# Kernel tuning notes

Hardware: AMD Instinct MI355X
Metric: run time of the kernel (lower is better)

The kernel has to match this reference:

```python
import jax, jax.numpy as jnp
import numpy as np

B, L, H, HEADS, DK = 256, 20, 128, 8, 16
NT, NR = 4, 4
CHILD, PARENT = 30001, 500
N1S, N1D, E1 = 50000, 20000, 300000
N2, E2 = 20000, 200000
T = B * L
N4D, E4 = 5000, 150000
EC2P = 8000
D2 = H // 2  # gamma=0.5 split for diachronic embedding


def _ln(x):
    m = jnp.mean(x, -1, keepdims=True)
    v = jnp.var(x, -1, keepdims=True)
    return (x - m) * jax.lax.rsqrt(v + 1e-5)


def _tmod(h, w, b):
    # temporal modulation with per-node diachronic params (activ='sin')
    return jnp.concatenate([h[..., :D2], h[..., D2:] * jnp.sin(w[..., D2:] + b[..., D2:])], -1)


def _dia(e, w, b, t):
    t = t[..., None].astype(e.dtype)
    return jnp.concatenate([e[..., :D2], e[..., D2:] * jnp.sin(w[..., D2:] * t + b[..., D2:])], -1)


def _typed(x, t, W):
    # type-conditioned linear: W [NT, in, out]; small NT -> compute all, select
    y = jnp.einsum('nh,tho->tno', x, W)
    return y[t, jnp.arange(x.shape[0])]


def _seg_softmax(s, seg, n):
    m = jax.ops.segment_max(s, seg, num_segments=n)
    m = jnp.where(jnp.isfinite(m), m, 0.0)
    ex = jnp.exp(s - m[seg])
    den = jax.ops.segment_sum(ex, seg, num_segments=n)
    return ex / jnp.maximum(den[seg], 1e-9)


def _htgt(src_h, src_t, tw, tb, eh, esrc, edst, etype, dst_h, dst_t, KW, QW, VW, OW, EW, mu):
    # relational multi-head attention on a bipartite block (HTGTLayer, pre_norm)
    nd = dst_h.shape[0]
    hs = _tmod(_ln(src_h), tw, tb)
    k = _typed(hs, src_t, KW).reshape(-1, HEADS, DK)
    v = _typed(hs, src_t, VW).reshape(-1, HEADS, DK)
    q = _typed(_ln(dst_h), dst_t, QW).reshape(nd, HEADS, DK)
    ke = k[esrc] + (eh @ EW).reshape(-1, HEADS, DK)
    score = (q[edst] * ke).sum(-1) * mu[etype] / np.float32(np.sqrt(DK))  # [E, HEADS]
    a = _seg_softmax(score, edst, nd)
    agg = jax.ops.segment_sum(a[..., None] * v[esrc], edst, num_segments=nd).reshape(nd, H)
    return _typed(agg, dst_t, OW) + dst_h


def _lstm(x, Wi, Wh, b):
    h0 = jnp.zeros((x.shape[0], H), x.dtype)
    def step(carry, xt):
        h, c = carry
        g = xt @ Wi + h @ Wh + b
        i, f, gg, o = jnp.split(g, 4, -1)
        c = jax.nn.sigmoid(f) * c + jax.nn.sigmoid(i) * jnp.tanh(gg)
        h = jax.nn.sigmoid(o) * jnp.tanh(c)
        return (h, c), h
    _, hs = jax.lax.scan(step, (h0, h0), jnp.swapaxes(x, 0, 1))
    return jnp.swapaxes(hs, 0, 1)


def _forward(seq, seq_ntype, dur, stime, etime, g1_nid, g1_ntype, g1_esrc, g1_edst, g1_etype, g1_ew,
             g2_src_sel, g2_esrc, g2_edst, g2_etype, g2_ew, tok_sel, g4_esrc, g4_edst, g4_etype, g4_ew,
             pe_p, pe_c, emb, hist_emb, edge_emb, dia_w, dia_b, t2v_w, t2v_b, exp_W, exp_b,
             lstm1_Wi, lstm1_Wh, lstm1_b, lstm2_Wi, lstm2_Wh, lstm2_b,
             convK, convQ, convV, convO, convE, convMu, ipW, iaW, skip):
    # ---- sequence module ----
    e0 = emb[seq]
    st = _dia(e0, dia_w[seq], dia_b[seq], stime)
    et = _dia(e0, dia_w[seq], dia_b[seq], etime)
    t = dur[..., None].astype(jnp.float32)
    tv = jnp.concatenate([t2v_w[:1] * t + t2v_b[:1], jnp.sin(t2v_w[1:] * t + t2v_b[1:])], -1)
    x = jax.nn.relu(jnp.concatenate([st, et, tv], -1) @ exp_W + exp_b)
    h1 = _lstm(x, lstm1_Wi, lstm1_Wh, lstm1_b)
    his = jnp.swapaxes(h1, 0, 1).reshape(T, H)  # packed (time-major) token states
    tok_id = jnp.swapaxes(seq, 0, 1).reshape(T)
    tok_nt = jnp.swapaxes(seq_ntype, 0, 1).reshape(T)
    # ---- conv1 (g2g) on block 1 ----
    sh1 = emb[g1_nid]
    xg = jax.nn.relu(_htgt(sh1, g1_ntype, dia_w[g1_nid], dia_b[g1_nid], edge_emb[g1_ew],
                           g1_esrc, g1_edst, g1_etype, sh1[:N1D], g1_ntype[:N1D],
                           convK[0], convQ[0], convV[0], convO[0], convE[0], convMu[0]))
    # ---- conv2 (g2s): graph nodes -> packed sequence tokens ----
    gnid2 = g1_nid[g2_src_sel]
    dst_h2 = xg[tok_sel] + his
    x2 = jax.nn.relu(_htgt(xg[g2_src_sel], g1_ntype[g2_src_sel], dia_w[gnid2], dia_b[gnid2], edge_emb[g2_ew],
                           g2_esrc, g2_edst, g2_etype, dst_h2, tok_nt,
                           convK[1], convQ[1], convV[1], convO[1], convE[1], convMu[1]))
    seq2 = jnp.swapaxes(x2.reshape(L, B, H), 0, 1)
    h2 = _lstm(seq2, lstm2_Wi, lstm2_Wh, lstm2_b)  # final seq_embed
    # ---- individual pooling (attn) + history push ----
    ent = jnp.swapaxes(h2, 0, 1).reshape(T, H)
    a = _typed(jnp.tanh(_typed(ent, tok_nt, ipW)), tok_nt, iaW)[:, 0]
    w = _seg_softmax(a, tok_id, CHILD)
    node_embed = jax.ops.segment_sum(w[:, None] * ent, tok_id, num_segments=CHILD)
    cnt = jax.ops.segment_sum(jnp.ones((T,), jnp.float32), tok_id, num_segments=CHILD)
    hist2 = jnp.where(cnt[:, None] > 0, node_embed, hist_emb)
    # ---- graph module: conv3, conv4 with skip-gated pull ----
    alpha = jax.nn.sigmoid(skip)[g1_ntype][:, None]
    x0 = emb[g1_nid] * alpha + hist2[g1_nid] * (1.0 - alpha)
    x3 = jax.nn.relu(_htgt(x0, g1_ntype, dia_w[g1_nid], dia_b[g1_nid], edge_emb[g1_ew],
                           g1_esrc, g1_edst, g1_etype, x0[:N1D], g1_ntype[:N1D],
                           convK[2], convQ[2], convV[2], convO[2], convE[2], convMu[2]))
    nid4 = g1_nid[:N1D]
    child_embed = _htgt(x3, g1_ntype[:N1D], dia_w[nid4], dia_b[nid4], edge_emb[g4_ew],
                        g4_esrc, g4_edst, g4_etype, x3[:N4D], g1_ntype[:N4D],
                        convK[3], convQ[3], convV[3], convO[3], convE[3], convMu[3])
    # ---- parent pooling (avg over c2p map) ----
    psum = jax.ops.segment_sum(child_embed[pe_c], pe_p, num_segments=PARENT)
    pcnt = jax.ops.segment_sum(jnp.ones((EC2P,), jnp.float32), pe_p, num_segments=PARENT)
    parent_embed = psum / jnp.maximum(pcnt, 1.0)[:, None]
    return (h2, child_embed, parent_embed)


def setup_inputs() -> dict:
    key = jax.random.key(0)
    ks = iter(jax.random.split(key, 64))
    def ri(shape, hi):
        return jax.random.randint(next(ks), shape, 0, hi, dtype=jnp.int32)
    def rn(shape, s=0.02):
        return jax.random.normal(next(ks), shape, dtype=jnp.float32) * s
    return dict(
        seq=ri((B, L), CHILD), seq_ntype=ri((B, L), NT), dur=ri((B, L), 40),
        stime=ri((B, L), 60), etime=ri((B, L), 60),
        g1_nid=ri((N1S,), CHILD), g1_ntype=ri((N1S,), NT),
        g1_esrc=ri((E1,), N1S), g1_edst=ri((E1,), N1D), g1_etype=ri((E1,), NR), g1_ew=ri((E1,), 50),
        g2_src_sel=ri((N2,), N1D), g2_esrc=ri((E2,), N2), g2_edst=ri((E2,), T),
        g2_etype=ri((E2,), NR), g2_ew=ri((E2,), 50),
        tok_sel=ri((T,), N1D),
        g4_esrc=ri((E4,), N1D), g4_edst=ri((E4,), N4D), g4_etype=ri((E4,), NR), g4_ew=ri((E4,), 50),
        pe_p=ri((EC2P,), PARENT), pe_c=ri((EC2P,), N4D),
        emb=rn((CHILD, H), 0.05), hist_emb=rn((CHILD, H), 0.05), edge_emb=rn((50, 32), 0.05),
        dia_w=rn((CHILD, H), 0.05), dia_b=rn((CHILD, H), 0.05),
        t2v_w=rn((16,), 0.1), t2v_b=rn((16,), 0.1),
        exp_W=rn((2 * H + 16, H)), exp_b=jnp.zeros((H,), jnp.float32),
        lstm1_Wi=rn((H, 4 * H)), lstm1_Wh=rn((H, 4 * H)), lstm1_b=jnp.zeros((4 * H,), jnp.float32),
        lstm2_Wi=rn((H, 4 * H)), lstm2_Wh=rn((H, 4 * H)), lstm2_b=jnp.zeros((4 * H,), jnp.float32),
        convK=rn((4, NT, H, H)), convQ=rn((4, NT, H, H)), convV=rn((4, NT, H, H)), convO=rn((4, NT, H, H)),
        convE=rn((4, 32, H)), convMu=jnp.ones((4, NR, HEADS), jnp.float32),
        ipW=rn((NT, H, H)), iaW=rn((NT, H, 1)), skip=jnp.ones((NT,), jnp.float32),
    )


def reference(seq, seq_ntype, dur, stime, etime, g1_nid, g1_ntype, g1_esrc, g1_edst, g1_etype, g1_ew,
              g2_src_sel, g2_esrc, g2_edst, g2_etype, g2_ew, tok_sel, g4_esrc, g4_edst, g4_etype, g4_ew,
              pe_p, pe_c, emb, hist_emb, edge_emb, dia_w, dia_b, t2v_w, t2v_b, exp_W, exp_b,
              lstm1_Wi, lstm1_Wh, lstm1_b, lstm2_Wi, lstm2_Wh, lstm2_b,
              convK, convQ, convV, convO, convE, convMu, ipW, iaW, skip):
    return _forward(seq, seq_ntype, dur, stime, etime, g1_nid, g1_ntype, g1_esrc, g1_edst, g1_etype, g1_ew,
                    g2_src_sel, g2_esrc, g2_edst, g2_etype, g2_ew, tok_sel, g4_esrc, g4_edst, g4_etype, g4_ew,
                    pe_p, pe_c, emb, hist_emb, edge_emb, dia_w, dia_b, t2v_w, t2v_b, exp_W, exp_b,
                    lstm1_Wi, lstm1_Wh, lstm1_b, lstm2_Wi, lstm2_Wh, lstm2_b,
                    convK, convQ, convV, convO, convE, convMu, ipW, iaW, skip)
```

## Files before the change

### kernel.cpp

```cpp
#include <hip/hip_runtime.h>
#include <math.h>

#define BB 256
#define LL 20
#define HH 128
#define NH 8
#define D2C 64
#define NTY 4
#define NRL 4
#define CHILDN 30001
#define PARENTN 500
#define N1SN 50000
#define N1DN 20000
#define E1N 300000
#define N2N 20000
#define E2N 200000
#define TT (BB*LL)
#define N4DN 5000
#define E4N 150000
#define EC2PN 8000
#define TDSTRIDE 2304

typedef __attribute__((ext_vector_type(8))) short bfrag;
typedef __attribute__((ext_vector_type(4))) float ffrag;
// ... 36 lines not shown
    const float* src = (fam==0?convK:fam==1?convV:fam==2?convQ:convO) + (size_t)lt*HH*HH;
    int j = im & 7, lane = (im>>3)&63, kc = (im>>9)&3, nt = im>>11;
    int k = kc*32 + (lane>>4)*8 + j;
    int n = nt*16 + (lane&15);
    Wsw[(size_t)m*16384 + im] = f2bf(src[k*HH+n]);
  }
  if(i < 4*16384){
    int m = i >> 14, im = i & 16383;
    const float* src = ipW + (size_t)m*HH*HH;
    int j = im & 7, lane = (im>>3)&63, kc = (im>>9)&3, nt = im>>11;
    int k = kc*32 + (lane>>4)*8 + j;
    int n = nt*16 + (lane&15);
    WswI[(size_t)m*16384 + im] = f2bf(src[k*HH+n]);
  }
  if(i < 4*50*HH){
    int layer = i/(50*HH), rr = (i/HH)%50, o = i%HH;
    const float* EWp = convE + (size_t)layer*32*HH;
    float acc = 0.f;
    for(int j=0;j<32;j++) acc += edge_emb[rr*32+j]*EWp[j*HH+o];
    EW2all[i] = acc;
  }
}

__global__ __launch_bounds__(512) void k_featx2(const int* __restrict__ seq, const int* __restrict__ dur,
                        const int* __restrict__ stime, const int* __restrict__ etime,
                        const float* __restrict__ emb, const float* __restrict__ dia_w, const float* __restrict__ dia_b,
                        const float* __restrict__ t2v_w, const float* __restrict__ t2v_b,
                        const float* __restrict__ exp_W, const float* __restrict__ exp_b, float* __restrict__ xout){
  __shared__ float feat[32*273];
  int base = blockIdx.x*32;
  int j = threadIdx.x >> 4;
  int p = threadIdx.x & 15;
  int row = base + j;
  int node = seq[row];
  float ts = (float)stime[row], te = (float)etime[row];
  const float* ep = emb + (size_t)node*HH;
  float* fr = feat + j*273;
  int o0 = p*8;
  #pragma unroll
  for(int ii=0; ii<8; ii+=4){
    int o = o0 + ii;
    float4 e = *(const float4*)(ep + o);
    float4 st = e, et = e;
    if(o >= D2C){
      float4 w = *(const float4*)(dia_w + (size_t)node*HH + o);
      float4 b = *(const float4*)(dia_b + (size_t)node*HH + o);
      st.x = e.x*__sinf(w.x*ts+b.x); st.y = e.y*__sinf(w.y*ts+b.y);
      st.z = e.z*__sinf(w.z*ts+b.z); st.w = e.w*__sinf(w.w*ts+b.w);
      et.x = e.x*__sinf(w.x*te+b.x); et.y = e.y*__sinf(w.y*te+b.y);
      et.z = e.z*__sinf(w.z*te+b.z); et.w = e.w*__sinf(w.w*te+b.w);
    }
    fr[o] = st.x; fr[o+1] = st.y; fr[o+2] = st.z; fr[o+3] = st.w;
    fr[128+o] = et.x; fr[128+o+1] = et.y; fr[128+o+2] = et.z; fr[128+o+3] = et.w;
  }
  if(p == 0){
    float td = (float)dur[row];
    #pragma unroll
    for(int i=0;i<16;i++){
      float w = t2v_w[i], b = t2v_b[i];
      fr[256+i] = (i==0) ? (w*td + b) : __sinf(w*td + b);
    }
  }
  __syncthreads();
  int oc = (threadIdx.x & 31)*4;
  int jg = threadIdx.x >> 5;
  const float* f0 = feat + (jg*2)*273;
  const float* f1 = feat + (jg*2+1)*273;
  float4 a0 = {0,0,0,0}, a1 = {0,0,0,0};
  for(int k=0;k<272;k++){
    float4 w = *(const float4*)(exp_W + (size_t)k*HH + oc);
    float x0 = f0[k], x1 = f1[k];
    a0.x += x0*w.x; a0.y += x0*w.y; a0.z += x0*w.z; a0.w += x0*w.w;
    a1.x += x1*w.x; a1.y += x1*w.y; a1.z += x1*w.z; a1.w += x1*w.w;
  }
  float4 bv = *(const float4*)(exp_b + oc);
  a0.x = fmaxf(a0.x+bv.x, 0.f); a0.y = fmaxf(a0.y+bv.y, 0.f);
  a0.z = fmaxf(a0.z+bv.z, 0.f); a0.w = fmaxf(a0.w+bv.w, 0.f);
  a1.x = fmaxf(a1.x+bv.x, 0.f); a1.y = fmaxf(a1.y+bv.y, 0.f);
  a1.z = fmaxf(a1.z+bv.z, 0.f); a1.w = fmaxf(a1.w+bv.w, 0.f);
  *(float4*)(xout + (size_t)(base + jg*2  )*HH + oc) = a0;
  *(float4*)(xout + (size_t)(base + jg*2+1)*HH + oc) = a1;
}

__global__ void k_xwi2(const float* x, const float* Wi, const float* bias, float* gpre, int rows, int perm){
  int base = blockIdx.x*16;
  __shared__ float xs[128*17];
  int tid = threadIdx.x;
  #pragma unroll
  for(int s=0;s<8;s++){
    int elem = tid + 256*s;
    int k = elem & 127, j = elem >> 7;
    int r = base + j;
    int src = r;
    if(perm) src = (r % LL)*BB + (r / LL);
    xs[k*17 + j] = (r < rows) ? x[(size_t)src*HH + k] : 0.f;
  }
  __syncthreads();
  int o4 = (tid & 127)*4;
  int ng = tid >> 7;
  float4 a[8];
  #pragma unroll
  for(int j=0;j<8;j++) a[j]=make_float4(0,0,0,0);
  for(int k=0;k<HH;k++){
    float4 w = *(const float4*)(Wi + (size_t)k*512 + o4);
    const float* xr = xs + k*17 + ng*8;
    #pragma unroll
    for(int j=0;j<8;j++){
      float xv = xr[j];
      a[j].x += xv*w.x; a[j].y += xv*w.y; a[j].z += xv*w.z; a[j].w += xv*w.w;
    }
  }
  float4 bv = *(const float4*)(bias + o4);
  #pragma unroll
  for(int j=0;j<8;j++){
    int r = base + ng*8 + j;
    if(r < rows){
      float4 v = a[j];
      v.x += bv.x; v.y += bv.y; v.z += bv.z; v.w += bv.w;
      *(float4*)(gpre + (size_t)r*512 + o4) = v;
    }
  }
}

__global__ __launch_bounds__(512, 2) void k_lstm_fused(const float* __restrict__ gpre,
                                                       const float* __restrict__ Wh,
                                                       float* __restrict__ hout,
                                                       float* __restrict__ hout2){
  int b = blockIdx.x;
  int o = threadIdx.x;
  __shared__ float hs[HH];
  __shared__ float act[512];
  float wr[HH];
  #pragma unroll
  for(int h=0;h<HH;h++) wr[h] = Wh[(size_t)h*512 + o];
  float gv[LL];
  const float* gp = gpre + (size_t)b*LL*512 + o;
  #pragma unroll
  for(int l=0;l<LL;l++) gv[l] = gp[(size_t)l*512];
  if(o < HH) hs[o] = 0.f;
  float cc = 0.f;
  int quad = o >> 7;
  __syncthreads();
  for(int l=0;l<LL;l++){
    float a0=0.f,a1=0.f,a2=0.f,a3=0.f;
    #pragma unroll
    for(int h=0;h<HH;h+=4){
      float4 hv = *(const float4*)&hs[h];
      a0 += hv.x*wr[h];   a1 += hv.y*wr[h+1];
      a2 += hv.z*wr[h+2]; a3 += hv.w*wr[h+3];
    }
    float g = gv[l] + ((a0+a1)+(a2+a3));
    act[o] = (quad==2) ? tanhfast(g) : sigfast(g);
    __syncthreads();
    if(o < HH){
      cc = act[HH+o]*cc + act[o]*act[2*HH+o];
      float hh = act[3*HH+o]*tanhfast(cc);
      hs[o] = hh;
      size_t bi = ((size_t)b*LL + l)*HH + o;
      hout[bi] = hh;
      if(hout2) hout2[bi] = hh;
    }
    __syncthreads();
  }
}

__global__ void k_scatall(const int* __restrict__ g1_nt, const int* __restrict__ seq,
                          const int* __restrict__ seq_nt, const int* __restrict__ g2_sel,
                          const int* __restrict__ g1_nid,
                          int* __restrict__ tokid, int* __restrict__ toknt, int* __restrict__ gnid2,
                          int* __restrict__ cntall,
                          int* __restrict__ idxS1, int* __restrict__ idxS2, int* __restrict__ idxS5,
                          int* __restrict__ idxS4, int* __restrict__ idxS3,
                          const int* __restrict__ e1d, int* __restrict__ icnt1, int* __restrict__ rank1,
                          const int* __restrict__ e2d, int* __restrict__ icnt2, int* __restrict__ rank2,
                          const int* __restrict__ e3d, int* __restrict__ icnt3, int* __restrict__ rank3){
  const int B1 = (N1SN+255)/256;
  const int B2 = (TT+255)/256;
  const int B3 = (N2N+255)/256;
  const int BE1 = (E1N+255)/256;
  const int BE2 = (E2N+255)/256;
  __shared__ int h[3][NTY];
  __shared__ int bs[3][NTY];
  int bx = blockIdx.x;
  if(bx < B1){
    int i = bx*256 + threadIdx.x;
    if(threadIdx.x < 3*NTY) (&h[0][0])[threadIdx.x] = 0;
    __syncthreads();
    int t = 0, r1 = 0, r2 = 0, r3 = 0;
    bool a1 = (i < N1SN), a2 = (i < N1DN), a3 = (i < N4DN);
    if(a1){
      t = g1_nt[i];
      r1 = atomicAdd(&h[0][t], 1);
      if(a2) r2 = atomicAdd(&h[1][t], 1);
      if(a3) r3 = atomicAdd(&h[2][t], 1);
    }
    __syncthreads();
    if(threadIdx.x < NTY){
      int ty = threadIdx.x;
      if(h[0][ty] > 0) bs[0][ty] = atomicAdd(&cntall[0*NTY+ty], h[0][ty]);
      if(h[1][ty] > 0) bs[1][ty] = atomicAdd(&cntall[1*NTY+ty], h[1][ty]);
      if(h[2][ty] > 0) bs[2][ty] = atomicAdd(&cntall[4*NTY+ty], h[2][ty]);
    }
    __syncthreads();
    if(a1) idxS1[t*N1SN + bs[0][t] + r1] = i;
    if(a2) idxS2[t*N1DN + bs[1][t] + r2] = i;
    if(a3) idxS5[t*N4DN + bs[2][t] + r3] = i;
  } else if(bx < B1 + B2){
    int i = (bx - B1)*256 + threadIdx.x;
    if(threadIdx.x < NTY) h[0][threadIdx.x] = 0;
    __syncthreads();
    int nt = 0, r = 0;
    bool act = (i < TT);
    if(act){
      int b = i % BB, l = i / BB;
      tokid[i] = seq[b*LL+l];
      nt = seq_nt[b*LL+l];
      toknt[i] = nt;
      r = atomicAdd(&h[0][nt], 1);
    }
    __syncthreads();
    if(threadIdx.x < NTY && h[0][threadIdx.x] > 0)
      bs[0][threadIdx.x] = atomicAdd(&cntall[3*NTY+threadIdx.x], h[0][threadIdx.x]);
    __syncthreads();
    if(act) idxS4[nt*TT + bs[0][nt] + r] = i;
  } else if(bx < B1 + B2 + B3){
    int i = (bx - B1 - B2)*256 + threadIdx.x;
    if(threadIdx.x < NTY) h[0][threadIdx.x] = 0;
    __syncthreads();
    int nt = 0, r = 0;
    bool act = (i < N2N);
    if(act){
      int s = g2_sel[i];
      gnid2[i] = g1_nid[s];
      nt = g1_nt[s];
      r = atomicAdd(&h[0][nt], 1);
    }
    __syncthreads();
    if(threadIdx.x < NTY && h[0][threadIdx.x] > 0)
      bs[0][threadIdx.x] = atomicAdd(&cntall[2*NTY+threadIdx.x], h[0][threadIdx.x]);
    __syncthreads();
    if(act) idxS3[nt*N2N + bs[0][nt] + r] = i;
  } else if(bx < B1 + B2 + B3 + BE1){
    int e = (bx - B1 - B2 - B3)*256 + threadIdx.x;
    if(e < E1N) rank1[e] = atomicAdd(&icnt1[e1d[e]], 1);
  } else if(bx < B1 + B2 + B3 + BE1 + BE2){
    int e = (bx - B1 - B2 - B3 - BE1)*256 + threadIdx.x;
    if(e < E2N) rank2[e] = atomicAdd(&icnt2[e2d[e]], 1);
  } else {
    int e = (bx - B1 - B2 - B3 - BE1 - BE2)*256 + threadIdx.x;
    if(e < E4N) rank3[e] = atomicAdd(&icnt3[e3d[e]], 1);
  }
}

__global__ void k_dst2(const int* tok_sel, const float* xg, const float* h1, float* dst2){
  int t = blockIdx.x; int o = threadIdx.x;
  int b = t % BB, l = t / BB;
  dst2[t*HH+o] = xg[tok_sel[t]*HH+o] + h1[(b*LL+l)*HH+o];
}

__global__ void k_x0(const int* nid, const int* ntype, const float* emb, const float* hist2,
                     const float* cnt, const float* hist_emb, const float* skip, float* srcbuf){
  int i = blockIdx.x; int o = threadIdx.x;
  float a = sigfast(skip[ntype[i]]);
  int nd = nid[i];
  float hv = (cnt[nd] > 0.f) ? hist2[(size_t)nd*HH+o] : hist_emb[(size_t)nd*HH+o];
  srcbuf[i*HH+o] = emb[(size_t)nd*HH+o]*a + hv*(1.f-a);
}

__global__ void k_mktiles(const int* __restrict__ cntall, int* __restrict__ tdesc, int* __restrict__ tcnt){
  __shared__ int start[3][2][NTY];
  if(threadIdx.x == 0){
    const int srcg[3] = {0,2,1};
    const int dstg[3] = {1,3,4};
    for(int c=0;c<3;c++){
      int acc = 0;
      for(int z=0;z<2;z++){
        int g = (z==0) ? srcg[c] : dstg[c];
        int zacc = 0;
        for(int t=0;t<NTY;t++){
          start[c][z][t] = acc;
          int tiles = (cntall[g*NTY+t]+31)>>5;
          acc += tiles; zacc += tiles;
        }
        tcnt[c*2+z] = zacc;
      }
    }
  }
  __syncthreads();
  const int srcg[3] = {0,2,1};
  const int dstg[3] = {1,3,4};
  for(int c=0;c<3;c++){
    for(int z=0;z<2;z++){
      int g = (z==0) ? srcg[c] : dstg[c];
      for(int t=0;t<NTY;t++){
        int tiles = (cntall[g*NTY+t]+31)>>5;
        for(int i=threadIdx.x; i<tiles; i+=blockDim.x)
          tdesc[c*TDSTRIDE + start[c][z][t] + i] = (int)(((unsigned)z<<31) | ((unsigned)t<<28) | (unsigned)(i<<5));
      }
    }
  }
}

__global__ __launch_bounds__(256) void k_gemm_kvq(
    const int* __restrict__ tdesc, const int* __restrict__ tcnt,
    const float* __restrict__ Xs, const int* __restrict__ src_nid, const int* __restrict__ smap,
    const float* __restrict__ sdia,
    const int* __restrict__ idxs, const int* __restrict__ cnts_s, int stride_s,
    const bfrag* __restrict__ WK, const bfrag* __restrict__ WV, unsigned* __restrict__ KVp,
    const float* __restrict__ Xq, const int* __restrict__ qmap,
    const int* __restrict__ idxd, const int* __restrict__ cnts_d, int stride_d,
    const bfrag* __restrict__ WQ, float* __restrict__ Qbuf){
  __shared__ float xs[32*132];
  __shared__ float mean_s[32], inv_s[32];
  __shared__ int sid[32], nid[32], xrow[32];
  int ntk = tcnt[0], ntq = tcnt[1];
  int bid = blockIdx.x;
  if(bid >= ntk + ntq) return;
  unsigned ud = (unsigned)tdesc[bid];
  int isQ = ud >> 31;
  int t = (ud >> 28) & 7;
  int base = ud & 0x0FFFFFFF;
  int tid = threadIdx.x;
  int cnt = isQ ? cnts_d[t] : cnts_s[t];
// ... 253 lines not shown
  for(int nt=0;nt<4;nt++){
    int col = (ng0+nt)*16 + col0;
    float wia = iaW[t*HH + col];
    #pragma unroll
    for(int i=0;i<4;i++) rsum[i] += tanhfast(acc[nt][i]) * wia;
  }
  #pragma unroll
  for(int i=0;i<4;i++){
    rsum[i] += __shfl_xor(rsum[i], 1, 64);
    rsum[i] += __shfl_xor(rsum[i], 2, 64);
    rsum[i] += __shfl_xor(rsum[i], 4, 64);
    rsum[i] += __shfl_xor(rsum[i], 8, 64);
  }
  if(col0 == 0){
    #pragma unroll
    for(int i=0;i<4;i++) atomicAdd(&red[rb+i], rsum[i]);
  }
  __syncthreads();
  if(tid < nn){
    int tok = sid[tid];
    float a = red[tid];
    abuf[tok] = a;
    atomicMax(&amax[tokid[tok]], fenc(a));
  }
}

__global__ void k_scan3(const int* c1, int n1, int* r1,
                        const int* c2, int n2, int* r2,
                        const int* c3, int n3, int* r3){
  __shared__ int tsum[1024];
  const int* cnt; int n; int* row_ptr;
  if(blockIdx.x == 0){ cnt=c1; n=n1; row_ptr=r1; }
  else if(blockIdx.x == 1){ cnt=c2; n=n2; row_ptr=r2; }
  else { cnt=c3; n=n3; row_ptr=r3; }
  int tid = threadIdx.x;
  int per = (n + 1023) / 1024;
  int start = tid*per; int end = min(start+per, n);
  int s = 0;
  for(int i=start;i<end;i++) s += cnt[i];
  tsum[tid] = s; __syncthreads();
  for(int off=1;off<1024;off<<=1){
    int v = (tid>=off) ? tsum[tid-off] : 0;
    __syncthreads();
    tsum[tid] += v;
    __syncthreads();
  }
  int run = (tid==0) ? 0 : tsum[tid-1];
  for(int i=start;i<end;i++){ row_ptr[i]=run; run += cnt[i]; }
  if(end == n) row_ptr[n] = run;
}
__global__ void k_fillperm3(const int* d1, const int* s1, const int* w1, const int* t1,
                            const int* rp1, const int* rk1, int2* m1,
                            const int* d2, const int* s2, const int* w2, const int* t2,
                            const int* rp2, const int* rk2, int2* m2,
                            const int* d3, const int* s3, const int* w3, const int* t3,
                            const int* rp3, const int* rk3, int2* m3){
  const int B1 = (E1N+255)/256, B2 = (E2N+255)/256;
  int bx = blockIdx.x;
  if(bx < B1){
    int e = bx*256 + threadIdx.x;
    if(e < E1N){ int pos = rp1[d1[e]] + rk1[e]; m1[pos] = make_int2(s1[e], w1[e] | (t1[e]<<16)); }
  } else if(bx < B1+B2){
    int e = (bx-B1)*256 + threadIdx.x;
    if(e < E2N){ int pos = rp2[d2[e]] + rk2[e]; m2[pos] = make_int2(s2[e], w2[e] | (t2[e]<<16)); }
  } else {
    int e = (bx-B1-B2)*256 + threadIdx.x;
    if(e < E4N){ int pos = rp3[d3[e]] + rk3[e]; m3[pos] = make_int2(s3[e], w3[e] | (t3[e]<<16)); }
  }
}

__global__ void k_attn_fused8(const int* __restrict__ row_ptr, const int2* __restrict__ meta,
                              const unsigned* __restrict__ KVp, const float* __restrict__ Qbuf,
                              const float* __restrict__ EW2, const float* __restrict__ mu,
                              float* __restrict__ Abuf){
  int d = blockIdx.x; int o = threadIdx.x;
  int r0 = row_ptr[d], r1 = row_ptr[d+1];
  __shared__ float q[HH];
  q[o] = Qbuf[(size_t)d*HH+o]*0.25f;
  __syncthreads();
  int h = o >> 4;
  float qo = q[o];
  float dn0=0.f, dn1=0.f, dn2=0.f, dn3=0.f;
  float ac0=0.f, ac1=0.f, ac2=0.f, ac3=0.f;
  int r = r0;
  for(; r+7 < r1; r += 8){
    int2 m[8]; unsigned u[8]; float e[8]; float p[8];
    #pragma unroll
    for(int j=0;j<8;j++) m[j] = meta[r+j];
    #pragma unroll
    for(int j=0;j<8;j++) u[j] = KVp[(size_t)m[j].x*HH + o];
// ... 207 lines not shown
    const bfrag* WK = WB + (size_t)( 0 + layer*4)*2048;
    const bfrag* WV = WB + (size_t)(16 + layer*4)*2048;
    const bfrag* WQ = WB + (size_t)(32 + layer*4)*2048;
    const bfrag* WO = WB + (size_t)(48 + layer*4)*2048;
    const float* MU  = convMu + (size_t)layer*NRL*NH;
    const float* EW2 = EW2all + (size_t)layer*50*HH;
    const int* td = tdesc + (size_t)cfg*TDSTRIDE;
    const int* tc = tcnt + cfg*2;
    k_gemm_kvq<<<gkvq, 256, 0, stream>>>(td, tc, src_X, src_nid, srcmap, sdia,
                                         idx_src, cnt_src, stride_src, WK, WV, KVp,
                                         q_X, q_map, idx_dst, cnt_dst, stride_dst, WQ, Qbuf);
    k_attn_fused8<<<ndst, HH, 0, stream>>>(rowp, meta, KVp, Qbuf, EW2, MU, Abuf);
    k_gemm_t5<<<gq, 256, 0, stream>>>(td, tc, Abuf, idx_dst, cnt_dst, stride_dst, WO,
                                      resid_X, r_map, outbuf, out2, relu);
  };

  k_init<<<(CHILDN*HH+255)/256, 256, 0, stream>>>(hist2, cnt, amax, aden, psum, pcnt, cntall,
                                                  icnt1, icnt2, icnt3,
                                                  dia_w, dia_b, sdia,
                                                  convK, convV, convQ, convO, Wsw,
                                                  ipW, WswI,
                                                  edge_emb, convE, EW2all);
  {
    const int B1 = (N1SN+255)/256, B2 = (TT+255)/256, B3 = (N2N+255)/256;
    const int BE1 = (E1N+255)/256, BE2 = (E2N+255)/256, BE3 = (E4N+255)/256;
    k_scatall<<<B1+B2+B3+BE1+BE2+BE3, 256, 0, stream>>>(g1_nt, seq, seq_nt, g2_sel, g1_nid,
                                            tokid, toknt, gnid2, cntall,
                                            idxS1, idxS2, idxS5, idxS4, idxS3,
                                            g1_edst, icnt1, g1rank,
                                            g2_edst, icnt2, g2rank,
                                            g4_edst, icnt3, g4rank);
  }
  k_mktiles<<<1, 256, 0, stream>>>(cntall, tdesc, tcnt);
  k_scan3<<<3, 1024, 0, stream>>>(icnt1, N1DN, g1row,
                                  icnt2, TT,   g2row,
                                  icnt3, N4DN, g4row);
  {
    const int BE1 = (E1N+255)/256, BE2 = (E2N+255)/256, BE3 = (E4N+255)/256;
    k_fillperm3<<<BE1+BE2+BE3, 256, 0, stream>>>(g1_edst, g1_esrc, g1_ew, g1_ety, g1row, g1rank, g1meta,
                                                 g2_edst, g2_esrc, g2_ew, g2_ety, g2row, g2rank, g2meta,
                                                 g4_edst, g4_esrc, g4_ew, g4_ety, g4row, g4rank, g4meta);
  }

  k_featx2<<<TT/32, 512, 0, stream>>>(seq, dur, stime, etime, emb, dia_w, dia_b, t2v_w, t2v_b, exp_W, exp_b, xbuf);
  k_xwi2<<<(TT+15)/16, 256, 0, stream>>>(xbuf, l1Wi, l1b, gpre, TT, 0);
  k_lstm_fused<<<BB, 512, 0, stream>>>(gpre, l1Wh, h1, (float*)nullptr);

  const int GKVQ_A = (N1SN+N1DN)/32 + 8;
  const int GKVQ_B = (N2N+TT)/32 + 8;
  const int GKVQ_C = (N1DN+N4DN)/32 + 8;
  const int GQ_A   = (N1DN+31)/32 + 4;
  const int GQ_B   = (TT+31)/32 + 4;
  const int GQ_C   = (N4DN+31)/32 + 4;

  run_conv(0, GKVQ_A, GQ_A,
           emb, g1_nid, g1_nid, idxS1, cntall+0*NTY, N1SN,
           emb, g1_nid,
           emb, g1_nid, N1DN, idxS2, cntall+1*NTY, N1DN,
           g1row, g1meta, 0, xg, (float*)nullptr, 1);

  k_dst2<<<TT, HH, 0, stream>>>(tok_sel, xg, h1, dst2);
  run_conv(1, GKVQ_B, GQ_B,
           xg, gnid2, g2_sel, idxS3, cntall+2*NTY, N2N,
           dst2, (const int*)nullptr,
           dst2, (const int*)nullptr, TT, idxS4, cntall+3*NTY, TT,
           g2row, g2meta, 1, x2, (float*)nullptr, 1);

  k_xwi2<<<(TT+15)/16, 256, 0, stream>>>(x2, l2Wi, l2b, gpre, TT, 1);
  k_lstm_fused<<<BB, 512, 0, stream>>>(gpre, l2Wh, h2f, outp);

  k_tokatt2<<<GQ_B, 256, 0, stream>>>(tdesc + (size_t)1*TDSTRIDE, tcnt + 2,
                                      h2f, idxS4, cntall+3*NTY,
                                      (const bfrag*)WswI, iaW, tokid, abuf, amax);
  k_tokexp<<<(TT+255)/256, 256, 0, stream>>>(tokid, abuf, amax, aden, cnt);
  k_tokagg<<<TT, HH, 0, stream>>>(tokid, abuf, aden, h2f, hist2);

  k_x0<<<N1SN, HH, 0, stream>>>(g1_nid, g1_nt, emb, hist2, cnt, hist_emb, skip, srcbuf);
  run_conv(0, GKVQ_A, GQ_A,
           srcbuf, g1_nid, (const int*)nullptr, idxS1, cntall+0*NTY, N1SN,
           srcbuf, (const int*)nullptr,
           srcbuf, (const int*)nullptr, N1DN, idxS2, cntall+1*NTY, N1DN,
           g1row, g1meta, 2, x3, (float*)nullptr, 1);

  run_conv(2, GKVQ_C, GQ_C,
           x3, g1_nid, (const int*)nullptr, idxS2, cntall+1*NTY, N1DN,
           x3, (const int*)nullptr,
           x3, (const int*)nullptr, N4DN, idxS5, cntall+4*NTY, N4DN,
           g4row, g4meta, 3, cef, outp + (size_t)TT*HH, 0);

  k_peagg<<<EC2PN, HH, 0, stream>>>(pe_p, pe_c, cef, psum, pcnt);
  k_parent<<<PARENTN, HH, 0, stream>>>(psum, pcnt, outp + (size_t)TT*HH + (size_t)N4DN*HH);
}
// ... 1 lines not shown
```

Measured before the change: 678.9 us.

## Merge independent preprocessing kernels into fewer multi-role launches

Folds the feature/expansion kernel and the index-scatter kernel into one launch, the input-projection GEMM together with the row-pointer scans and tile-descriptor build into a second, and the CSR fill into extra blocks of the first LSTM launch. This reduces the kernel launch count and the serialization gaps between small kernels by running independent work side by side. The scan now uses 256 threads instead of 1024, and the scatter blocks process 512 elements each. The mixed-role blocks share register and LDS budgets, which could lower occupancy for the heavier roles.

New measurement: 672.9 us. No clear change (-0.9%).

```diff
diff --git a/kernel.cpp b/kernel.cpp
--- a/kernel.cpp
+++ b/kernel.cpp
@@ -82,168 +82,90 @@
   }
 }
 
-__global__ __launch_bounds__(512) void k_featx2(const int* __restrict__ seq, const int* __restrict__ dur,
-                        const int* __restrict__ stime, const int* __restrict__ etime,
-                        const float* __restrict__ emb, const float* __restrict__ dia_w, const float* __restrict__ dia_b,
-                        const float* __restrict__ t2v_w, const float* __restrict__ t2v_b,
-                        const float* __restrict__ exp_W, const float* __restrict__ exp_b, float* __restrict__ xout){
-  __shared__ float feat[32*273];
-  int base = blockIdx.x*32;
-  int j = threadIdx.x >> 4;
-  int p = threadIdx.x & 15;
-  int row = base + j;
-  int node = seq[row];
-  float ts = (float)stime[row], te = (float)etime[row];
-  const float* ep = emb + (size_t)node*HH;
-  float* fr = feat + j*273;
-  int o0 = p*8;
-  #pragma unroll
-  for(int ii=0; ii<8; ii+=4){
-    int o = o0 + ii;
-    float4 e = *(const float4*)(ep + o);
-    float4 st = e, et = e;
-    if(o >= D2C){
-      float4 w = *(const float4*)(dia_w + (size_t)node*HH + o);
-      float4 b = *(const float4*)(dia_b + (size_t)node*HH + o);
-      st.x = e.x*__sinf(w.x*ts+b.x); st.y = e.y*__sinf(w.y*ts+b.y);
-      st.z = e.z*__sinf(w.z*ts+b.z); st.w = e.w*__sinf(w.w*ts+b.w);
-      et.x = e.x*__sinf(w.x*te+b.x); et.y = e.y*__sinf(w.y*te+b.y);
-      et.z = e.z*__sinf(w.z*te+b.z); et.w = e.w*__sinf(w.w*te+b.w);
-    }
-    fr[o] = st.x; fr[o+1] = st.y; fr[o+2] = st.z; fr[o+3] = st.w;
-    fr[128+o] = et.x; fr[128+o+1] = et.y; fr[128+o+2] = et.z; fr[128+o+3] = et.w;
-  }
-  if(p == 0){
-    float td = (float)dur[row];
-    #pragma unroll
-    for(int i=0;i<16;i++){
-      float w = t2v_w[i], b = t2v_b[i];
-      fr[256+i] = (i==0) ? (w*td + b) : __sinf(w*td + b);
-    }
-  }
-  __syncthreads();
-  int oc = (threadIdx.x & 31)*4;
-  int jg = threadIdx.x >> 5;
-  const float* f0 = feat + (jg*2)*273;
-  const float* f1 = feat + (jg*2+1)*273;
-  float4 a0 = {0,0,0,0}, a1 = {0,0,0,0};
-  for(int k=0;k<272;k++){
-    float4 w = *(const float4*)(exp_W + (size_t)k*HH + oc);
-    float x0 = f0[k], x1 = f1[k];
-    a0.x += x0*w.x; a0.y += x0*w.y; a0.z += x0*w.z; a0.w += x0*w.w;
-    a1.x += x1*w.x; a1.y += x1*w.y; a1.z += x1*w.z; a1.w += x1*w.w;
-  }
-  float4 bv = *(const float4*)(exp_b + oc);
-  a0.x = fmaxf(a0.x+bv.x, 0.f); a0.y = fmaxf(a0.y+bv.y, 0.f);
-  a0.z = fmaxf(a0.z+bv.z, 0.f); a0.w = fmaxf(a0.w+bv.w, 0.f);
-  a1.x = fmaxf(a1.x+bv.x, 0.f); a1.y = fmaxf(a1.y+bv.y, 0.f);
-  a1.z = fmaxf(a1.z+bv.z, 0.f); a1.w = fmaxf(a1.w+bv.w, 0.f);
-  *(float4*)(xout + (size_t)(base + jg*2  )*HH + oc) = a0;
-  *(float4*)(xout + (size_t)(base + jg*2+1)*HH + oc) = a1;
-}
-
-__global__ void k_xwi2(const float* x, const float* Wi, const float* bias, float* gpre, int rows, int perm){
-  int base = blockIdx.x*16;
-  __shared__ float xs[128*17];
-  int tid = threadIdx.x;
-  #pragma unroll
-  for(int s=0;s<8;s++){
-    int elem = tid + 256*s;
-    int k = elem & 127, j = elem >> 7;
-    int r = base + j;
-    int src = r;
-    if(perm) src = (r % LL)*BB + (r / LL);
-    xs[k*17 + j] = (r < rows) ? x[(size_t)src*HH + k] : 0.f;
-  }
-  __syncthreads();
-  int o4 = (tid & 127)*4;
-  int ng = tid >> 7;
-  float4 a[8];
-  #pragma unroll
-  for(int j=0;j<8;j++) a[j]=make_float4(0,0,0,0);
-  for(int k=0;k<HH;k++){
-    float4 w = *(const float4*)(Wi + (size_t)k*512 + o4);
-    const float* xr = xs + k*17 + ng*8;
-    #pragma unroll
-    for(int j=0;j<8;j++){
-      float xv = xr[j];
-      a[j].x += xv*w.x; a[j].y += xv*w.y; a[j].z += xv*w.z; a[j].w += xv*w.w;
-    }
-  }
-  float4 bv = *(const float4*)(bias + o4);
-  #pragma unroll
-  for(int j=0;j<8;j++){
-    int r = base + ng*8 + j;
-    if(r < rows){
-      float4 v = a[j];
-      v.x += bv.x; v.y += bv.y; v.z += bv.z; v.w += bv.w;
-      *(float4*)(gpre + (size_t)r*512 + o4) = v;
-    }
-  }
-}
-
-__global__ __launch_bounds__(512, 2) void k_lstm_fused(const float* __restrict__ gpre,
-                                                       const float* __restrict__ Wh,
-                                                       float* __restrict__ hout,
-                                                       float* __restrict__ hout2){
-  int b = blockIdx.x;
-  int o = threadIdx.x;
-  __shared__ float hs[HH];
-  __shared__ float act[512];
-  float wr[HH];
-  #pragma unroll
-  for(int h=0;h<HH;h++) wr[h] = Wh[(size_t)h*512 + o];
-  float gv[LL];
-  const float* gp = gpre + (size_t)b*LL*512 + o;
-  #pragma unroll
-  for(int l=0;l<LL;l++) gv[l] = gp[(size_t)l*512];
-  if(o < HH) hs[o] = 0.f;
-  float cc = 0.f;
-  int quad = o >> 7;
-  __syncthreads();
-  for(int l=0;l<LL;l++){
-    float a0=0.f,a1=0.f,a2=0.f,a3=0.f;
-    #pragma unroll
-    for(int h=0;h<HH;h+=4){
-      float4 hv = *(const float4*)&hs[h];
-      a0 += hv.x*wr[h];   a1 += hv.y*wr[h+1];
-      a2 += hv.z*wr[h+2]; a3 += hv.w*wr[h+3];
-    }
-    float g = gv[l] + ((a0+a1)+(a2+a3));
-    act[o] = (quad==2) ? tanhfast(g) : sigfast(g);
-    __syncthreads();
-    if(o < HH){
-      cc = act[HH+o]*cc + act[o]*act[2*HH+o];
-      float hh = act[3*HH+o]*tanhfast(cc);
-      hs[o] = hh;
-      size_t bi = ((size_t)b*LL + l)*HH + o;
-      hout[bi] = hh;
-      if(hout2) hout2[bi] = hh;
-    }
-    __syncthreads();
-  }
-}
-
-__global__ void k_scatall(const int* __restrict__ g1_nt, const int* __restrict__ seq,
-                          const int* __restrict__ seq_nt, const int* __restrict__ g2_sel,
-                          const int* __restrict__ g1_nid,
-                          int* __restrict__ tokid, int* __restrict__ toknt, int* __restrict__ gnid2,
-                          int* __restrict__ cntall,
-                          int* __restrict__ idxS1, int* __restrict__ idxS2, int* __restrict__ idxS5,
-                          int* __restrict__ idxS4, int* __restrict__ idxS3,
-                          const int* __restrict__ e1d, int* __restrict__ icnt1, int* __restrict__ rank1,
-                          const int* __restrict__ e2d, int* __restrict__ icnt2, int* __restrict__ rank2,
-                          const int* __restrict__ e3d, int* __restrict__ icnt3, int* __restrict__ rank3){
-  const int B1 = (N1SN+255)/256;
-  const int B2 = (TT+255)/256;
-  const int B3 = (N2N+255)/256;
-  const int BE1 = (E1N+255)/256;
-  const int BE2 = (E2N+255)/256;
+#define S1_BF   (TT/32)
+#define S1_B1   ((N1SN+511)/512)
+#define S1_B2   ((TT+511)/512)
+#define S1_B3   ((N2N+511)/512)
+#define S1_BE1  ((E1N+511)/512)
+#define S1_BE2  ((E2N+511)/512)
+#define S1_BE3  ((E4N+511)/512)
+__global__ __launch_bounds__(512) void k_stage1(
+    const int* __restrict__ seq, const int* __restrict__ dur,
+    const int* __restrict__ stime, const int* __restrict__ etime,
+    const float* __restrict__ emb, const float* __restrict__ dia_w, const float* __restrict__ dia_b,
+    const float* __restrict__ t2v_w, const float* __restrict__ t2v_b,
+    const float* __restrict__ exp_W, const float* __restrict__ exp_b, float* __restrict__ xout,
+    const int* __restrict__ g1_nt, const int* __restrict__ seq_nt, const int* __restrict__ g2_sel,
+    const int* __restrict__ g1_nid,
+    int* __restrict__ tokid, int* __restrict__ toknt, int* __restrict__ gnid2,
+    int* __restrict__ cntall,
+    int* __restrict__ idxS1, int* __restrict__ idxS2, int* __restrict__ idxS5,
+    int* __restrict__ idxS4, int* __restrict__ idxS3,
+    const int* __restrict__ e1d, int* __restrict__ icnt1, int* __restrict__ rank1,
+    const int* __restrict__ e2d, int* __restrict__ icnt2, int* __restrict__ rank2,
+    const int* __restrict__ e3d, int* __restrict__ icnt3, int* __restrict__ rank3){
+  int bxx = blockIdx.x;
+  if(bxx < S1_BF){
+    __shared__ float feat[32*273];
+    int base = bxx*32;
+    int j = threadIdx.x >> 4;
+    int p = threadIdx.x & 15;
+    int row = base + j;
+    int node = seq[row];
+    float ts = (float)stime[row], te = (float)etime[row];
+    const float* ep = emb + (size_t)node*HH;
+    float* fr = feat + j*273;
+    int o0 = p*8;
+    #pragma unroll
+    for(int ii=0; ii<8; ii+=4){
+      int o = o0 + ii;
+      float4 e = *(const float4*)(ep + o);
+      float4 st = e, et = e;
+      if(o >= D2C){
+        float4 w = *(const float4*)(dia_w + (size_t)node*HH + o);
+        float4 b = *(const float4*)(dia_b + (size_t)node*HH + o);
+        st.x = e.x*__sinf(w.x*ts+b.x); st.y = e.y*__sinf(w.y*ts+b.y);
+        st.z = e.z*__sinf(w.z*ts+b.z); st.w = e.w*__sinf(w.w*ts+b.w);
+        et.x = e.x*__sinf(w.x*te+b.x); et.y = e.y*__sinf(w.y*te+b.y);
+        et.z = e.z*__sinf(w.z*te+b.z); et.w = e.w*__sinf(w.w*te+b.w);
+      }
+      fr[o] = st.x; fr[o+1] = st.y; fr[o+2] = st.z; fr[o+3] = st.w;
+      fr[128+o] = et.x; fr[128+o+1] = et.y; fr[128+o+2] = et.z; fr[128+o+3] = et.w;
+    }
+    if(p == 0){
+      float td = (float)dur[row];
+      #pragma unroll
+      for(int i=0;i<16;i++){
+        float w = t2v_w[i], b = t2v_b[i];
+        fr[256+i] = (i==0) ? (w*td + b) : __sinf(w*td + b);
+      }
+    }
+    __syncthreads();
+    int oc = (threadIdx.x & 31)*4;
+    int jg = threadIdx.x >> 5;
+    const float* f0 = feat + (jg*2)*273;
+    const float* f1 = feat + (jg*2+1)*273;
+    float4 a0 = {0,0,0,0}, a1 = {0,0,0,0};
+    for(int k=0;k<272;k++){
+      float4 w = *(const float4*)(exp_W + (size_t)k*HH + oc);
+      float x0 = f0[k], x1 = f1[k];
+      a0.x += x0*w.x; a0.y += x0*w.y; a0.z += x0*w.z; a0.w += x0*w.w;
+      a1.x += x1*w.x; a1.y += x1*w.y; a1.z += x1*w.z; a1.w += x1*w.w;
+    }
+    float4 bv = *(const float4*)(exp_b + oc);
+    a0.x = fmaxf(a0.x+bv.x, 0.f); a0.y = fmaxf(a0.y+bv.y, 0.f);
+    a0.z = fmaxf(a0.z+bv.z, 0.f); a0.w = fmaxf(a0.w+bv.w, 0.f);
+    a1.x = fmaxf(a1.x+bv.x, 0.f); a1.y = fmaxf(a1.y+bv.y, 0.f);
+    a1.z = fmaxf(a1.z+bv.z, 0.f); a1.w = fmaxf(a1.w+bv.w, 0.f);
+    *(float4*)(xout + (size_t)(base + jg*2  )*HH + oc) = a0;
+    *(float4*)(xout + (size_t)(base + jg*2+1)*HH + oc) = a1;
+    return;
+  }
   __shared__ int h[3][NTY];
   __shared__ int bs[3][NTY];
-  int bx = blockIdx.x;
-  if(bx < B1){
-    int i = bx*256 + threadIdx.x;
+  int bx = bxx - S1_BF;
+  if(bx < S1_B1){
+    int i = bx*512 + threadIdx.x;
     if(threadIdx.x < 3*NTY) (&h[0][0])[threadIdx.x] = 0;
     __syncthreads();
     int t = 0, r1 = 0, r2 = 0, r3 = 0;
@@ -265,8 +187,8 @@
     if(a1) idxS1[t*N1SN + bs[0][t] + r1] = i;
     if(a2) idxS2[t*N1DN + bs[1][t] + r2] = i;
     if(a3) idxS5[t*N4DN + bs[2][t] + r3] = i;
-  } else if(bx < B1 + B2){
-    int i = (bx - B1)*256 + threadIdx.x;
+  } else if(bx < S1_B1 + S1_B2){
+    int i = (bx - S1_B1)*512 + threadIdx.x;
     if(threadIdx.x < NTY) h[0][threadIdx.x] = 0;
     __syncthreads();
     int nt = 0, r = 0;
@@ -283,8 +205,8 @@
       bs[0][threadIdx.x] = atomicAdd(&cntall[3*NTY+threadIdx.x], h[0][threadIdx.x]);
     __syncthreads();
     if(act) idxS4[nt*TT + bs[0][nt] + r] = i;
-  } else if(bx < B1 + B2 + B3){
-    int i = (bx - B1 - B2)*256 + threadIdx.x;
+  } else if(bx < S1_B1 + S1_B2 + S1_B3){
+    int i = (bx - S1_B1 - S1_B2)*512 + threadIdx.x;
     if(threadIdx.x < NTY) h[0][threadIdx.x] = 0;
     __syncthreads();
     int nt = 0, r = 0;
@@ -300,15 +222,185 @@
       bs[0][threadIdx.x] = atomicAdd(&cntall[2*NTY+threadIdx.x], h[0][threadIdx.x]);
     __syncthreads();
     if(act) idxS3[nt*N2N + bs[0][nt] + r] = i;
-  } else if(bx < B1 + B2 + B3 + BE1){
-    int e = (bx - B1 - B2 - B3)*256 + threadIdx.x;
+  } else if(bx < S1_B1 + S1_B2 + S1_B3 + S1_BE1){
+    int e = (bx - S1_B1 - S1_B2 - S1_B3)*512 + threadIdx.x;
     if(e < E1N) rank1[e] = atomicAdd(&icnt1[e1d[e]], 1);
-  } else if(bx < B1 + B2 + B3 + BE1 + BE2){
-    int e = (bx - B1 - B2 - B3 - BE1)*256 + threadIdx.x;
+  } else if(bx < S1_B1 + S1_B2 + S1_B3 + S1_BE1 + S1_BE2){
+    int e = (bx - S1_B1 - S1_B2 - S1_B3 - S1_BE1)*512 + threadIdx.x;
     if(e < E2N) rank2[e] = atomicAdd(&icnt2[e2d[e]], 1);
   } else {
-    int e = (bx - B1 - B2 - B3 - BE1 - BE2)*256 + threadIdx.x;
+    int e = (bx - S1_B1 - S1_B2 - S1_B3 - S1_BE1 - S1_BE2)*512 + threadIdx.x;
     if(e < E4N) rank3[e] = atomicAdd(&icnt3[e3d[e]], 1);
+  }
+}
+
+__device__ __forceinline__ void scan_one(const int* cnt, int n, int* row_ptr){
+  __shared__ int tsum[256];
+  int tid = threadIdx.x;
+  int per = (n + 255) / 256;
+  int start = tid*per; int end = min(start+per, n);
+  int s = 0;
+  for(int i=start;i<end;i++) s += cnt[i];
+  tsum[tid] = s; __syncthreads();
+  for(int off=1;off<256;off<<=1){
+    int v = (tid>=off) ? tsum[tid-off] : 0;
+    __syncthreads();
+    tsum[tid] += v;
+    __syncthreads();
+  }
+  int run = (tid==0) ? 0 : tsum[tid-1];
+  for(int i=start;i<end;i++){ row_ptr[i]=run; run += cnt[i]; }
+  if(end == n) row_ptr[n] = run;
+}
+
+__global__ __launch_bounds__(256) void k_stage2(
+    const float* x, const float* Wi, const float* bias, float* gpre, int rows, int perm,
+    const int* c1, int* r1, const int* c2, int* r2, const int* c3, int* r3,
+    const int* __restrict__ cntall, int* __restrict__ tdesc, int* __restrict__ tcnt){
+  int nxwi = (rows+15)/16;
+  int bxx = blockIdx.x;
+  if(bxx < nxwi){
+    int base = bxx*16;
+    __shared__ float xs[128*17];
+    int tid = threadIdx.x;
+    #pragma unroll
+    for(int s=0;s<8;s++){
+      int elem = tid + 256*s;
+      int k = elem & 127, j = elem >> 7;
+      int r = base + j;
+      int src = r;
+      if(perm) src = (r % LL)*BB + (r / LL);
+      xs[k*17 + j] = (r < rows) ? x[(size_t)src*HH + k] : 0.f;
+    }
+    __syncthreads();
+    int o4 = (tid & 127)*4;
+    int ng = tid >> 7;
+    float4 a[8];
+    #pragma unroll
+    for(int j=0;j<8;j++) a[j]=make_float4(0,0,0,0);
+    for(int k=0;k<HH;k++){
+      float4 w = *(const float4*)(Wi + (size_t)k*512 + o4);
+      const float* xr = xs + k*17 + ng*8;
+      #pragma unroll
+      for(int j=0;j<8;j++){
+        float xv = xr[j];
+        a[j].x += xv*w.x; a[j].y += xv*w.y; a[j].z += xv*w.z; a[j].w += xv*w.w;
+      }
+    }
+    float4 bv = *(const float4*)(bias + o4);
+    #pragma unroll
+    for(int j=0;j<8;j++){
+      int r = base + ng*8 + j;
+      if(r < rows){
+        float4 v = a[j];
+        v.x += bv.x; v.y += bv.y; v.z += bv.z; v.w += bv.w;
+        *(float4*)(gpre + (size_t)r*512 + o4) = v;
+      }
+    }
+    return;
+  }
+  int bx = bxx - nxwi;
+  if(bx == 0){ scan_one(c1, N1DN, r1); }
+  else if(bx == 1){ scan_one(c2, TT, r2); }
+  else if(bx == 2){ scan_one(c3, N4DN, r3); }
+  else {
+    __shared__ int start[3][2][NTY];
+    if(threadIdx.x == 0){
+      const int srcg[3] = {0,2,1};
+      const int dstg[3] = {1,3,4};
+      for(int c=0;c<3;c++){
+        int acc = 0;
+        for(int z=0;z<2;z++){
+          int g = (z==0) ? srcg[c] : dstg[c];
+          int zacc = 0;
+          for(int t=0;t<NTY;t++){
+            start[c][z][t] = acc;
+            int tiles = (cntall[g*NTY+t]+31)>>5;
+            acc += tiles; zacc += tiles;
+          }
+          tcnt[c*2+z] = zacc;
+        }
+      }
+    }
+    __syncthreads();
+    const int srcg[3] = {0,2,1};
+    const int dstg[3] = {1,3,4};
+    for(int c=0;c<3;c++){
+      for(int z=0;z<2;z++){
+        int g = (z==0) ? srcg[c] : dstg[c];
+        for(int t=0;t<NTY;t++){
+          int tiles = (cntall[g*NTY+t]+31)>>5;
+          for(int i=threadIdx.x; i<tiles; i+=blockDim.x)
+            tdesc[c*TDSTRIDE + start[c][z][t] + i] = (int)(((unsigned)z<<31) | ((unsigned)t<<28) | (unsigned)(i<<5));
+        }
+      }
+    }
+  }
+}
+
+#define LF_BE1 ((E1N+511)/512)
+#define LF_BE2 ((E2N+511)/512)
+#define LF_BE3 ((E4N+511)/512)
+__global__ __launch_bounds__(512, 2) void k_lstm_fused(const float* __restrict__ gpre,
+                                                       const float* __restrict__ Wh,
+                                                       float* __restrict__ hout,
+                                                       float* __restrict__ hout2,
+    const int* d1, const int* s1, const int* w1, const int* t1,
+    const int* rp1, const int* rk1, int2* m1,
+    const int* d2, const int* s2, const int* w2, const int* t2,
+    const int* rp2, const int* rk2, int2* m2,
+    const int* d3, const int* s3, const int* w3, const int* t3,
+    const int* rp3, const int* rk3, int2* m3){
+  if(blockIdx.x >= BB){
+    int bx = blockIdx.x - BB;
+    int tid = threadIdx.x;
+    if(bx < LF_BE1){
+      int e = bx*512 + tid;
+      if(e < E1N){ int pos = rp1[d1[e]] + rk1[e]; m1[pos] = make_int2(s1[e], w1[e] | (t1[e]<<16)); }
+    } else if(bx < LF_BE1 + LF_BE2){
+      int e = (bx - LF_BE1)*512 + tid;
+      if(e < E2N){ int pos = rp2[d2[e]] + rk2[e]; m2[pos] = make_int2(s2[e], w2[e] | (t2[e]<<16)); }
+    } else {
+      int e = (bx - LF_BE1 - LF_BE2)*512 + tid;
+      if(e < E4N){ int pos = rp3[d3[e]] + rk3[e]; m3[pos] = make_int2(s3[e], w3[e] | (t3[e]<<16)); }
+    }
+    return;
+  }
+  int b = blockIdx.x;
+  int o = threadIdx.x;
+  __shared__ float hs[HH];
+  __shared__ float act[512];
+  float wr[HH];
+  #pragma unroll
+  for(int h=0;h<HH;h++) wr[h] = Wh[(size_t)h*512 + o];
+  float gv[LL];
+  const float* gp = gpre + (size_t)b*LL*512 + o;
+  #pragma unroll
+  for(int l=0;l<LL;l++) gv[l] = gp[(size_t)l*512];
+  if(o < HH) hs[o] = 0.f;
+  float cc = 0.f;
+  int quad = o >> 7;
+  __syncthreads();
+  for(int l=0;l<LL;l++){
+    float a0=0.f,a1=0.f,a2=0.f,a3=0.f;
+    #pragma unroll
+    for(int h=0;h<HH;h+=4){
+      float4 hv = *(const float4*)&hs[h];
+      a0 += hv.x*wr[h];   a1 += hv.y*wr[h+1];
+      a2 += hv.z*wr[h+2]; a3 += hv.w*wr[h+3];
+    }
+    float g = gv[l] + ((a0+a1)+(a2+a3));
+    act[o] = (quad==2) ? tanhfast(g) : sigfast(g);
+    __syncthreads();
+    if(o < HH){
+      cc = act[HH+o]*cc + act[o]*act[2*HH+o];
+      float hh = act[3*HH+o]*tanhfast(cc);
+      hs[o] = hh;
+      size_t bi = ((size_t)b*LL + l)*HH + o;
+      hout[bi] = hh;
+      if(hout2) hout2[bi] = hh;
+    }
+    __syncthreads();
   }
 }
 
@@ -325,40 +417,6 @@
   int nd = nid[i];
   float hv = (cnt[nd] > 0.f) ? hist2[(size_t)nd*HH+o] : hist_emb[(size_t)nd*HH+o];
   srcbuf[i*HH+o] = emb[(size_t)nd*HH+o]*a + hv*(1.f-a);
-}
-
-__global__ void k_mktiles(const int* __restrict__ cntall, int* __restrict__ tdesc, int* __restrict__ tcnt){
-  __shared__ int start[3][2][NTY];
-  if(threadIdx.x == 0){
-    const int srcg[3] = {0,2,1};
-    const int dstg[3] = {1,3,4};
-    for(int c=0;c<3;c++){
-      int acc = 0;
-      for(int z=0;z<2;z++){
-        int g = (z==0) ? srcg[c] : dstg[c];
-        int zacc = 0;
-        for(int t=0;t<NTY;t++){
-          start[c][z][t] = acc;
-          int tiles = (cntall[g*NTY+t]+31)>>5;
-          acc += tiles; zacc += tiles;
-        }
-        tcnt[c*2+z] = zacc;
-      }
-    }
-  }
-  __syncthreads();
-  const int srcg[3] = {0,2,1};
-  const int dstg[3] = {1,3,4};
-  for(int c=0;c<3;c++){
-    for(int z=0;z<2;z++){
-      int g = (z==0) ? srcg[c] : dstg[c];
-      for(int t=0;t<NTY;t++){
-        int tiles = (cntall[g*NTY+t]+31)>>5;
-        for(int i=threadIdx.x; i<tiles; i+=blockDim.x)
-          tdesc[c*TDSTRIDE + start[c][z][t] + i] = (int)(((unsigned)z<<31) | ((unsigned)t<<28) | (unsigned)(i<<5));
-      }
-    }
-  }
 }
 
 __global__ __launch_bounds__(256) void k_gemm_kvq(
@@ -658,50 +716,6 @@
     float a = red[tid];
     abuf[tok] = a;
     atomicMax(&amax[tokid[tok]], fenc(a));
-  }
-}
-
-__global__ void k_scan3(const int* c1, int n1, int* r1,
-                        const int* c2, int n2, int* r2,
-                        const int* c3, int n3, int* r3){
-  __shared__ int tsum[1024];
-  const int* cnt; int n; int* row_ptr;
-  if(blockIdx.x == 0){ cnt=c1; n=n1; row_ptr=r1; }
-  else if(blockIdx.x == 1){ cnt=c2; n=n2; row_ptr=r2; }
-  else { cnt=c3; n=n3; row_ptr=r3; }
-  int tid = threadIdx.x;
-  int per = (n + 1023) / 1024;
-  int start = tid*per; int end = min(start+per, n);
-  int s = 0;
-  for(int i=start;i<end;i++) s += cnt[i];
-  tsum[tid] = s; __syncthreads();
-  for(int off=1;off<1024;off<<=1){
-    int v = (tid>=off) ? tsum[tid-off] : 0;
-    __syncthreads();
-    tsum[tid] += v;
-    __syncthreads();
-  }
-  int run = (tid==0) ? 0 : tsum[tid-1];
-  for(int i=start;i<end;i++){ row_ptr[i]=run; run += cnt[i]; }
-  if(end == n) row_ptr[n] = run;
-}
-__global__ void k_fillperm3(const int* d1, const int* s1, const int* w1, const int* t1,
-                            const int* rp1, const int* rk1, int2* m1,
-                            const int* d2, const int* s2, const int* w2, const int* t2,
-                            const int* rp2, const int* rk2, int2* m2,
-                            const int* d3, const int* s3, const int* w3, const int* t3,
-                            const int* rp3, const int* rk3, int2* m3){
-  const int B1 = (E1N+255)/256, B2 = (E2N+255)/256;
-  int bx = blockIdx.x;
-  if(bx < B1){
-    int e = bx*256 + threadIdx.x;
-    if(e < E1N){ int pos = rp1[d1[e]] + rk1[e]; m1[pos] = make_int2(s1[e], w1[e] | (t1[e]<<16)); }
-  } else if(bx < B1+B2){
-    int e = (bx-B1)*256 + threadIdx.x;
-    if(e < E2N){ int pos = rp2[d2[e]] + rk2[e]; m2[pos] = make_int2(s2[e], w2[e] | (t2[e]<<16)); }
-  } else {
-    int e = (bx-B1-B2)*256 + threadIdx.x;
-    if(e < E4N){ int pos = rp3[d3[e]] + rk3[e]; m3[pos] = make_int2(s3[e], w3[e] | (t3[e]<<16)); }
   }
 }
 
@@ -955,29 +969,23 @@
                                                   ipW, WswI,
                                                   edge_emb, convE, EW2all);
   {
-    const int B1 = (N1SN+255)/256, B2 = (TT+255)/256, B3 = (N2N+255)/256;
-    const int BE1 = (E1N+255)/256, BE2 = (E2N+255)/256, BE3 = (E4N+255)/256;
-    k_scatall<<<B1+B2+B3+BE1+BE2+BE3, 256, 0, stream>>>(g1_nt, seq, seq_nt, g2_sel, g1_nid,
-                                            tokid, toknt, gnid2, cntall,
-                                            idxS1, idxS2, idxS5, idxS4, idxS3,
-                                            g1_edst, icnt1, g1rank,
-                                            g2_edst, icnt2, g2rank,
-                                            g4_edst, icnt3, g4rank);
-  }
-  k_mktiles<<<1, 256, 0, stream>>>(cntall, tdesc, tcnt);
-  k_scan3<<<3, 1024, 0, stream>>>(icnt1, N1DN, g1row,
-                                  icnt2, TT,   g2row,
-                                  icnt3, N4DN, g4row);
-  {
-    const int BE1 = (E1N+255)/256, BE2 = (E2N+255)/256, BE3 = (E4N+255)/256;
-    k_fillperm3<<<BE1+BE2+BE3, 256, 0, stream>>>(g1_edst, g1_esrc, g1_ew, g1_ety, g1row, g1rank, g1meta,
-                                                 g2_edst, g2_esrc, g2_ew, g2_ety, g2row, g2rank, g2meta,
-                                                 g4_edst, g4_esrc, g4_ew, g4_ety, g4row, g4rank, g4meta);
-  }
-
-  k_featx2<<<TT/32, 512, 0, stream>>>(seq, dur, stime, etime, emb, dia_w, dia_b, t2v_w, t2v_b, exp_W, exp_b, xbuf);
-  k_xwi2<<<(TT+15)/16, 256, 0, stream>>>(xbuf, l1Wi, l1b, gpre, TT, 0);
-  k_lstm_fused<<<BB, 512, 0, stream>>>(gpre, l1Wh, h1, (float*)nullptr);
+    const int G1 = S1_BF + S1_B1 + S1_B2 + S1_B3 + S1_BE1 + S1_BE2 + S1_BE3;
+    k_stage1<<<G1, 512, 0, stream>>>(seq, dur, stime, etime, emb, dia_w, dia_b,
+                                     t2v_w, t2v_b, exp_W, exp_b, xbuf,
+                                     g1_nt, seq_nt, g2_sel, g1_nid,
+                                     tokid, toknt, gnid2, cntall,
+                                     idxS1, idxS2, idxS5, idxS4, idxS3,
+                                     g1_edst, icnt1, g1rank,
+                                     g2_edst, icnt2, g2rank,
+                                     g4_edst, icnt3, g4rank);
+  }
+  k_stage2<<<(TT+15)/16 + 4, 256, 0, stream>>>(xbuf, l1Wi, l1b, gpre, TT, 0,
+                                               icnt1, g1row, icnt2, g2row, icnt3, g4row,
+                                               cntall, tdesc, tcnt);
+  k_lstm_fused<<<BB + LF_BE1 + LF_BE2 + LF_BE3, 512, 0, stream>>>(gpre, l1Wh, h1, (float*)nullptr,
+      g1_edst, g1_esrc, g1_ew, g1_ety, g1row, g1rank, g1meta,
+      g2_edst, g2_esrc, g2_ew, g2_ety, g2row, g2rank, g2meta,
+      g4_edst, g4_esrc, g4_ew, g4_ety, g4row, g4rank, g4meta);
 
   const int GKVQ_A = (N1SN+N1DN)/32 + 8;
   const int GKVQ_B = (N2N+TT)/32 + 8;
@@ -999,8 +1007,13 @@
            dst2, (const int*)nullptr, TT, idxS4, cntall+3*NTY, TT,
            g2row, g2meta, 1, x2, (float*)nullptr, 1);
 
-  k_xwi2<<<(TT+15)/16, 256, 0, stream>>>(x2, l2Wi, l2b, gpre, TT, 1);
-  k_lstm_fused<<<BB, 512, 0, stream>>>(gpre, l2Wh, h2f, outp);
+  k_stage2<<<(TT+15)/16, 256, 0, stream>>>(x2, l2Wi, l2b, gpre, TT, 1,
+                                           icnt1, g1row, icnt2, g2row, icnt3, g4row,
+                                           cntall, tdesc, tcnt);
+  k_lstm_fused<<<BB, 512, 0, stream>>>(gpre, l2Wh, h2f, outp,
+      g1_edst, g1_esrc, g1_ew, g1_ety, g1row, g1rank, g1meta,
+      g2_edst, g2_esrc, g2_ew, g2_ety, g2row, g2rank, g2meta,
+      g4_edst, g4_esrc, g4_ew, g4_ety, g4row, g4rank, g4meta);
 
   k_tokatt2<<<GQ_B, 256, 0, stream>>>(tdesc + (size_t)1*TDSTRIDE, tcnt + 2,
                                       h2f, idxS4, cntall+3*NTY,
```
